# Kernel tuning notes

Measured on AMD Instinct MI355X. Metric: run time of the kernel, lower is better.

## Reference

```python
import jax, jax.numpy as jnp
import numpy as np
from jax import lax

B, L, DDYN, DSTAT, H = 512, 64, 16, 8, 512
N_BANK, C_CAND, K_TOP, N_PROTO = 50000, 1024, 16, 8
T_TARG, Q_QUANT = 2, 3
TEMP = 0.2


def _l2norm(x, eps=1e-12):
    # matches torch.nn.functional.normalize: x / max(||x||, eps)
    n = jnp.sqrt(jnp.sum(x * x, axis=-1, keepdims=True))
    return x / jnp.maximum(n, eps)


def setup_inputs() -> dict:
    key = jax.random.key(0)
    ks = jax.random.split(key, 24)
    s = 0.02
    inp = {
        'sequence_values': jax.random.normal(ks[0], (B, L, DDYN), jnp.float32),
        'sequence_masks': jnp.ones((B, L), jnp.float32),
        'static_values': jax.random.normal(ks[1], (B, DSTAT), jnp.float32),
        'bank_keys': jax.random.normal(ks[2], (N_BANK, H), jnp.float32),
        'bank_values': jax.random.normal(ks[3], (N_BANK, H), jnp.float32),
        'candidate_indices': jax.random.randint(ks[4], (B, C_CAND), 0, N_BANK, jnp.int64),
        # encoder params (SequenceEncoder stand-in: masked-mean + linear + relu)
        'W_seq': jax.random.normal(ks[5], (DDYN, H), jnp.float32) * s,
        'W_stat': jax.random.normal(ks[6], (DSTAT, H), jnp.float32) * s,
        'b_enc': jnp.zeros((H,), jnp.float32),
        # retrieval / prototype / fusion params
        'W_q': jax.random.normal(ks[7], (H, H), jnp.float32) * s,
        'b_q': jnp.zeros((H,), jnp.float32),
        'prototype_tokens': jax.random.normal(ks[8], (N_PROTO, H), jnp.float32) * 0.02,
        'W_tr': jax.random.normal(ks[9], (2 * H, H), jnp.float32) * s,
        'b_tr': jnp.zeros((H,), jnp.float32),
        'W_gate': jax.random.normal(ks[10], (3 * H, H), jnp.float32) * s,
        'b_gate': jnp.zeros((H,), jnp.float32),
        'W_out': jax.random.normal(ks[11], (H, H), jnp.float32) * s,
        'b_out': jnp.zeros((H,), jnp.float32),
        # per-target heads stacked: [T, H, Q] and [T, H]
        'W_quant': jax.random.normal(ks[12], (T_TARG, H, Q_QUANT), jnp.float32) * s,
        'b_quant': jnp.zeros((T_TARG, Q_QUANT), jnp.float32),
        'W_ev': jax.random.normal(ks[13], (T_TARG, H), jnp.float32) * s,
        'b_ev': jnp.zeros((T_TARG,), jnp.float32),
    }
    return inp


def reference(sequence_values, sequence_masks, static_values, bank_keys, bank_values,
              candidate_indices, W_seq, W_stat, b_enc, W_q, b_q, prototype_tokens,
              W_tr, b_tr, W_gate, b_gate, W_out, b_out, W_quant, b_quant, W_ev, b_ev):
    # --- encoder (masked mean pool + linear + relu stand-in for SequenceEncoder) ---
    m = sequence_masks[..., None]                                   # [B,L,1]
    pooled = (sequence_values * m).sum(1) / jnp.maximum(m.sum(1), 1e-6)
    local_hidden = jax.nn.relu(pooled @ W_seq + static_values @ W_stat + b_enc)  # [B,H]

    # --- normalized query ---
    query = _l2norm(local_hidden @ W_q + b_q)                       # [B,H]

    # --- donor retrieval: gather + dot + topk + softmax + weighted sum ---
    cand_keys = bank_keys[candidate_indices]                        # [B,C,H]
    sim = jnp.einsum('bch,bh->bc', cand_keys, query)                # [B,C]
    top_scores, top_pos = lax.top_k(sim, K_TOP)                     # [B,K]
    weights = jax.nn.softmax(top_scores / max(TEMP, 1e-6), axis=-1)
    sel_idx = jnp.take_along_axis(candidate_indices, top_pos, axis=1)  # [B,K]
    donor_hidden = jnp.einsum('bk,bkh->bh', weights, bank_values[sel_idx])

    # --- prototype attention ---
    protos_n = _l2norm(prototype_tokens)                            # [P,H]
    pw = jax.nn.softmax(query @ protos_n.T, axis=-1)                # [B,P]
    proto_hidden = pw @ prototype_tokens                            # [B,H]

    # --- transfer / gate / fuse (dropout is identity at eval) ---
    transfer = jax.nn.relu(jnp.concatenate([donor_hidden, proto_hidden], -1) @ W_tr + b_tr)
    gate = jax.nn.sigmoid(
        jnp.concatenate([local_hidden, donor_hidden, proto_hidden], -1) @ W_gate + b_gate)
    fused = gate * local_hidden + (1.0 - gate) * transfer
    fused = jax.nn.relu(fused @ W_out + b_out)                      # [B,H]

    # --- heads: sorted quantiles [B,T,Q] and event logits [B,T] ---
    quant = jnp.sort(jnp.einsum('bh,thq->btq', fused, W_quant) + b_quant, axis=-1)
    logit = jnp.einsum('bh,th->bt', fused, W_ev) + b_ev
    return jnp.concatenate([quant.reshape(quant.shape[0], -1), logit], axis=-1)  # [B, T*Q+T]
```

## Files before the change

kernel.cpp:

```cpp
#include <hip/hip_runtime.h>
#include <hip/hip_bf16.h>

typedef __hip_bfloat16 bf16;

__device__ __forceinline__ float lo16(unsigned u){ return __uint_as_float(u << 16); }
__device__ __forceinline__ float hi16(unsigned u){ return __uint_as_float(u & 0xffff0000u); }

#define Bn 512
#define Hn 512
#define Cn 1024
#define Kn 16
#define NBANK 50000

__device__ __forceinline__ int clamp_id(int id){
    return (id < 0) ? 0 : ((id >= NBANK) ? (NBANK - 1) : id);
}

#define QRAW_OFF 0
#define F1_OFF   0
#define G_OFF    262144
#define SIM_OFF  1048576
#define F2_OFF   1048576
#define GATE_OFF 1572864
#define TR_OFF   1835008
#define WS_FLOATS 2097152

__global__ __launch_bounds__(256) void k_enc(
    const float* __restrict__ seq, const float* __restrict__ mask, const float* __restrict__ stat,
    const float* __restrict__ W_seq, const float* __restrict__ W_stat, const float* __restrict__ b_enc,
    float* __restrict__ ws)
{
    const int b = blockIdx.x, t = threadIdx.x;
    const int h0 = 2*t, h1 = 2*t + 1;
    __shared__ float s_pool[16], s_stat[8];
    if (t < 16) {
        float acc = 0.f, ms = 0.f;
        for (int l = 0; l < 64; l++) {
            float m = mask[b*64 + l];
            ms  += m;
            acc += seq[(b*64 + l)*16 + t] * m;
        }
        s_pool[t] = acc / fmaxf(ms, 1e-6f);
    } else if (t < 24) {
        s_stat[t - 16] = stat[b*8 + (t - 16)];
    }
    __syncthreads();
    float a0 = b_enc[h0], a1 = b_enc[h1];
    #pragma unroll
    for (int j = 0; j < 16; j++) {
        float2 wv = *(const float2*)(W_seq + j*Hn + h0);
        a0 += s_pool[j]*wv.x; a1 += s_pool[j]*wv.y;
    }
    #pragma unroll
    for (int j = 0; j < 8; j++) {
        float2 wv = *(const float2*)(W_stat + j*Hn + h0);
        a0 += s_stat[j]*wv.x; a1 += s_stat[j]*wv.y;
    }
    float* g = ws + G_OFF + (size_t)b*1536;
    g[h0] = fmaxf(a0, 0.f); g[h1] = fmaxf(a1, 0.f);
}

__global__ __launch_bounds__(256) void k_qgemm_sk(
    const float* __restrict__ W, const float* __restrict__ bias,
    const float* __restrict__ in, int in_stride, int in_off,
    float* __restrict__ outp)
{
    const int ct = blockIdx.x, rt = blockIdx.y, kz = blockIdx.z, t = threadIdx.x;
    __shared__ float lt[64][132];
    {
        int r = t >> 2, c0 = (t & 3)*32;
        const float* src = in + (size_t)(rt*64 + r)*in_stride + in_off + kz*128 + c0;
        #pragma unroll
        for (int i = 0; i < 8; i++)
            *(float4*)&lt[r][c0 + i*4] = *(const float4*)(src + i*4);
    }
    __syncthreads();
    const int col0 = ct*64 + (t & 15)*4, rbase = (t >> 4)*4;
    float acc[4][4];
    if (kz == 0) {
        float4 bv = *(const float4*)(bias + col0);
        #pragma unroll
        for (int i = 0; i < 4; i++) { acc[i][0]=bv.x; acc[i][1]=bv.y; acc[i][2]=bv.z; acc[i][3]=bv.w; }
    } else {
        #pragma unroll
        for (int i = 0; i < 4; i++) { acc[i][0]=0; acc[i][1]=0; acc[i][2]=0; acc[i][3]=0; }
    }
    const float* wp = W + (size_t)(kz*128)*Hn + col0;
    #pragma unroll 4
    for (int k = 0; k < 128; k++) {
        float4 wv = *(const float4*)(wp + (size_t)k*Hn);
        #pragma unroll
        for (int i = 0; i < 4; i++) {
            float a = lt[rbase + i][k];
            acc[i][0] += a*wv.x; acc[i][1] += a*wv.y; acc[i][2] += a*wv.z; acc[i][3] += a*wv.w;
        }
    }
    #pragma unroll
    for (int i = 0; i < 4; i++) {
        float* op = outp + (size_t)(rt*64 + rbase + i)*Hn + col0;
        atomicAdd(op+0, acc[i][0]); atomicAdd(op+1, acc[i][1]);
        atomicAdd(op+2, acc[i][2]); atomicAdd(op+3, acc[i][3]);
    }
}

__global__ __launch_bounds__(256) void k_sim(
    const float* __restrict__ bank_keys, const int* __restrict__ cand32,
    float* __restrict__ ws)
{
    const int chunk = blockIdx.x, b = blockIdx.y, t = threadIdx.x;
    const int w = t >> 6, lane = t & 63;
    const int c64 = ((cand32[1] | cand32[3] | cand32[5] | cand32[7]) == 0) ? 1 : 0;

    const float* qr = ws + QRAW_OFF + (size_t)b*Hn + lane*8;
    float4 qa = *(const float4*)qr, qb = *(const float4*)(qr + 4);
    float ss = qa.x*qa.x + qa.y*qa.y + qa.z*qa.z + qa.w*qa.w
             + qb.x*qb.x + qb.y*qb.y + qb.z*qb.z + qb.w*qb.w;
    #pragma unroll
    for (int o = 32; o; o >>= 1) ss += __shfl_xor(ss, o);
    float inv = 1.f / fmaxf(sqrtf(ss), 1e-12f);
    float qv[8] = {qa.x*inv, qa.y*inv, qa.z*inv, qa.w*inv,
                   qb.x*inv, qb.y*inv, qb.z*inv, qb.w*inv};

    const int cbase = b*Cn + chunk*128 + w*32;
    float* simrow = ws + SIM_OFF + (size_t)b*Cn + chunk*128 + w*32;
    for (int g8 = 0; g8 < 32; g8 += 8) {
        float4 ka[8], kb2[8];
        #pragma unroll
        for (int u = 0; u < 8; u++) {
            int id = clamp_id(cand32[(size_t)(cbase + g8 + u) << c64]);
            const float* kp = bank_keys + (size_t)id*Hn + lane*8;
            ka[u]  = *(const float4*)kp;
            kb2[u] = *(const float4*)(kp + 4);
        }
        #pragma unroll
        for (int u = 0; u < 8; u++) {
            float s = ka[u].x*qv[0] + ka[u].y*qv[1] + ka[u].z*qv[2] + ka[u].w*qv[3]
                    + kb2[u].x*qv[4] + kb2[u].y*qv[5] + kb2[u].z*qv[6] + kb2[u].w*qv[7];
            #pragma unroll
            for (int o = 32; o; o >>= 1) s += __shfl_xor(s, o);
            if (lane == 0) simrow[g8 + u] = s;
        }
    }
}

__global__ __launch_bounds__(256) void k_select(
    const float* __restrict__ bank_values, const int* __restrict__ cand32,
    const float* __restrict__ proto, float* __restrict__ ws)
{
    const int b = blockIdx.x, t = threadIdx.x;
    const int w = t >> 6, lane = t & 63;
    const int h0 = 2*t, h1 = 2*t + 1;
    const int c64 = ((cand32[1] | cand32[3] | cand32[5] | cand32[7]) == 0) ? 1 : 0;

    __shared__ __align__(16) float s_sim[Cn];
    __shared__ float s_bv[4]; __shared__ int s_bi[4];
    __shared__ float s_topv[Kn]; __shared__ int s_sel[Kn];
    __shared__ float s_w[Kn];
    __shared__ float s_score[8], s_pw[8];

    *(float4*)&s_sim[t*4] = *(const float4*)(ws + SIM_OFF + (size_t)b*Cn + t*4);

    const float* qr = ws + QRAW_OFF + (size_t)b*Hn + lane*8;
    float4 qa = *(const float4*)qr, qb = *(const float4*)(qr + 4);
    float ss = qa.x*qa.x + qa.y*qa.y + qa.z*qa.z + qa.w*qa.w
             + qb.x*qb.x + qb.y*qb.y + qb.z*qb.z + qb.w*qb.w;
    #pragma unroll
    for (int o = 32; o; o >>= 1) ss += __shfl_xor(ss, o);
    float qinv = 1.f / fmaxf(sqrtf(ss), 1e-12f);
    float qv[8] = {qa.x*qinv, qa.y*qinv, qa.z*qinv, qa.w*qinv,
                   qb.x*qinv, qb.y*qinv, qb.z*qinv, qb.w*qinv};
    __syncthreads();

    for (int k = 0; k < Kn; k++) {
        float best = -1e30f; int bi = 0x7fffffff;
        for (int i = t; i < Cn; i += 256) {
            float v = s_sim[i];
            if (v > best || (v == best && i < bi)) { best = v; bi = i; }
        }
        #pragma unroll
        for (int o = 32; o; o >>= 1) {
            float ov = __shfl_xor(best, o); int oi = __shfl_xor(bi, o);
            if (ov > best || (ov == best && oi < bi)) { best = ov; bi = oi; }
        }
        if (lane == 0) { s_bv[w] = best; s_bi[w] = bi; }
        __syncthreads();
        if (t == 0) {
            float bv = s_bv[0]; int bbi = s_bi[0];
            for (int x = 1; x < 4; x++)
                if (s_bv[x] > bv || (s_bv[x] == bv && s_bi[x] < bbi)) { bv = s_bv[x]; bbi = s_bi[x]; }
            if (bbi < 0 || bbi >= Cn) bbi = 0;
            s_topv[k] = bv; s_sel[k] = bbi; s_sim[bbi] = -1e30f;
        }
        __syncthreads();
    }

    if (t == 0) {
        float m = s_topv[0];
        float e[Kn], ssum = 0.f;
        for (int k = 0; k < Kn; k++) { e[k] = __expf((s_topv[k] - m) * 5.0f); ssum += e[k]; }
        float inv = 1.f / ssum;
        for (int k = 0; k < Kn; k++) s_w[k] = e[k] * inv;
    }
    for (int p = w; p < 8; p += 4) {
        const float* pp = proto + (size_t)p*Hn + lane*8;
        float4 pa = *(const float4*)pp, pb = *(const float4*)(pp + 4);
        float f[8] = {pa.x, pa.y, pa.z, pa.w, pb.x, pb.y, pb.z, pb.w};
        float dq = 0.f, sq = 0.f;
        #pragma unroll
        for (int i = 0; i < 8; i++) { dq += f[i]*qv[i]; sq += f[i]*f[i]; }
        #pragma unroll
        for (int o = 32; o; o >>= 1) { dq += __shfl_xor(dq, o); sq += __shfl_xor(sq, o); }
        if (lane == 0) s_score[p] = dq / fmaxf(sqrtf(sq), 1e-12f);
    }
    __syncthreads();
    if (t == 0) {
        float m = s_score[0];
        for (int p = 1; p < 8; p++) m = fmaxf(m, s_score[p]);
        float e[8], ssum = 0.f;
        for (int p = 0; p < 8; p++) { e[p] = __expf(s_score[p] - m); ssum += e[p]; }
        float inv = 1.f / ssum;
        for (int p = 0; p < 8; p++) s_pw[p] = e[p] * inv;
    }
    __syncthreads();

    float* g = ws + G_OFF + (size_t)b*1536;
    {
        float a0 = 0.f, a1 = 0.f;
        #pragma unroll
        for (int k = 0; k < Kn; k++) {
            int id = clamp_id(cand32[(size_t)(b*Cn + s_sel[k]) << c64]);
            float2 v = *(const float2*)(bank_values + (size_t)id*Hn + h0);
            a0 += s_w[k]*v.x; a1 += s_w[k]*v.y;
        }
        g[512 + h0] = a0; g[512 + h1] = a1;
    }
    {
        float a0 = 0.f, a1 = 0.f;
        #pragma unroll
        for (int p = 0; p < 8; p++) {
            float2 v = *(const float2*)(proto + (size_t)p*Hn + h0);
            a0 += s_pw[p]*v.x; a1 += s_pw[p]*v.y;
        }
        g[1024 + h0] = a0; g[1024 + h1] = a1;
    }
}

__global__ __launch_bounds__(256) void k_gatetr_sk(
    const float* __restrict__ W_tr, const float* __restrict__ b_tr,
    const float* __restrict__ W_gate, const float* __restrict__ b_gate,
    float* __restrict__ ws)
{
    const int ct = blockIdx.x, rt = blockIdx.y, z = blockIdx.z, t = threadIdx.x;
    const int isGate = (z < 6);
    const int slice = isGate ? z : (z - 6);
    const float* W  = isGate ? W_gate : W_tr;
    const int inoff = (isGate ? 0 : 512) + slice*256;
    float* outp = ws + (isGate ? GATE_OFF : TR_OFF);

    __shared__ float lt[32][260];
    {
        int r = t >> 3, c0 = (t & 7)*32;
        const float* src = ws + G_OFF + (size_t)(rt*32 + r)*1536 + inoff + c0;
        #pragma unroll
        for (int i = 0; i < 8; i++)
            *(float4*)&lt[r][c0 + i*4] = *(const float4*)(src + i*4);
    }
    __syncthreads();
    const int col0 = ct*128 + (t & 31)*4, rbase = (t >> 5)*4;
    float acc[4][4];
    if (slice == 0) {
        const float* bias = isGate ? b_gate : b_tr;
        float4 bv = *(const float4*)(bias + col0);
        #pragma unroll
        for (int i = 0; i < 4; i++) { acc[i][0]=bv.x; acc[i][1]=bv.y; acc[i][2]=bv.z; acc[i][3]=bv.w; }
    } else {
        #pragma unroll
        for (int i = 0; i < 4; i++) { acc[i][0]=0; acc[i][1]=0; acc[i][2]=0; acc[i][3]=0; }
    }
    const float* wp = W + (size_t)(slice*256)*Hn + col0;
    #pragma unroll 4
    for (int k = 0; k < 256; k++) {
        float4 wv = *(const float4*)(wp + (size_t)k*Hn);
        #pragma unroll
        for (int i = 0; i < 4; i++) {
            float a = lt[rbase + i][k];
            acc[i][0] += a*wv.x; acc[i][1] += a*wv.y; acc[i][2] += a*wv.z; acc[i][3] += a*wv.w;
        }
    }
    #pragma unroll
    for (int i = 0; i < 4; i++) {
        float* op = outp + (size_t)(rt*32 + rbase + i)*Hn + col0;
        atomicAdd(op+0, acc[i][0]); atomicAdd(op+1, acc[i][1]);
        atomicAdd(op+2, acc[i][2]); atomicAdd(op+3, acc[i][3]);
    }
}

__global__ __launch_bounds__(256) void k_f1ew(float* __restrict__ ws)
{
    const int i4 = blockIdx.x*256 + threadIdx.x;
    const int row = i4 >> 7, c = (i4 & 127)*4;
    float4 lc = *(const float4*)(ws + G_OFF + (size_t)row*1536 + c);
    float4 ga = *(const float4*)(ws + GATE_OFF + (size_t)row*Hn + c);
    float4 tr = *(const float4*)(ws + TR_OFF + (size_t)row*Hn + c);
    float4 r;
    float s;
    s = 1.f/(1.f + __expf(-ga.x)); r.x = s*lc.x + (1.f-s)*fmaxf(tr.x, 0.f);
    s = 1.f/(1.f + __expf(-ga.y)); r.y = s*lc.y + (1.f-s)*fmaxf(tr.y, 0.f);
    s = 1.f/(1.f + __expf(-ga.z)); r.z = s*lc.z + (1.f-s)*fmaxf(tr.z, 0.f);
    s = 1.f/(1.f + __expf(-ga.w)); r.w = s*lc.w + (1.f-s)*fmaxf(tr.w, 0.f);
    *(float4*)(ws + F1_OFF + (size_t)row*Hn + c) = r;
}

__global__ __launch_bounds__(64) void k_heads(
    const float* __restrict__ W_quant, const float* __restrict__ b_quant,
    const float* __restrict__ W_ev, const float* __restrict__ b_ev,
    const float* __restrict__ ws_ro, float* __restrict__ out)
{
    const int b = blockIdx.x, lane = threadIdx.x;
    const float* fr = ws_ro + F2_OFF + (size_t)b*Hn + lane*8;
    float4 fa = *(const float4*)fr, fb = *(const float4*)(fr + 4);
    float fv[8] = {fmaxf(fa.x,0.f), fmaxf(fa.y,0.f), fmaxf(fa.z,0.f), fmaxf(fa.w,0.f),
                   fmaxf(fb.x,0.f), fmaxf(fb.y,0.f), fmaxf(fb.z,0.f), fmaxf(fb.w,0.f)};
    float acc[8];
    #pragma unroll
    for (int o = 0; o < 8; o++) acc[o] = 0.f;
    #pragma unroll
    for (int i = 0; i < 8; i++) {
        int h = lane*8 + i;
        float fh = fv[i];
        acc[0] += fh*W_quant[(0*Hn + h)*3 + 0];
        acc[1] += fh*W_quant[(0*Hn + h)*3 + 1];
        acc[2] += fh*W_quant[(0*Hn + h)*3 + 2];
        acc[3] += fh*W_quant[(1*Hn + h)*3 + 0];
        acc[4] += fh*W_quant[(1*Hn + h)*3 + 1];
        acc[5] += fh*W_quant[(1*Hn + h)*3 + 2];
        acc[6] += fh*W_ev[0*Hn + h];
        acc[7] += fh*W_ev[1*Hn + h];
    }
    #pragma unroll
    for (int o = 0; o < 8; o++) {
        #pragma unroll
        for (int s = 32; s; s >>= 1) acc[o] += __shfl_xor(acc[o], s);
    }
    if (lane == 0) {
        float q[6];
        for (int o = 0; o < 6; o++) q[o] = acc[o] + b_quant[o];
        #pragma unroll
        for (int tt = 0; tt < 2; tt++) {
            float a = q[tt*3], bb = q[tt*3+1], c = q[tt*3+2];
            float mn = fminf(a, fminf(bb, c)), mx = fmaxf(a, fmaxf(bb, c));
            float md = a + bb + c - mn - mx;
            q[tt*3] = mn; q[tt*3+1] = md; q[tt*3+2] = mx;
        }
        for (int o = 0; o < 6; o++) out[b*8 + o] = q[o];
        out[b*8 + 6] = acc[6] + b_ev[0];
        out[b*8 + 7] = acc[7] + b_ev[1];
    }
}

__device__ __forceinline__ float lds_f(const void* p, int i, int f32){
    return f32 ? ((const float*)p)[i] : __bfloat162float(((const bf16*)p)[i]);
}
__device__ __forceinline__ float2 ldpair(const void* p, int elt, int f32){
    if (f32) return ((const float2*)p)[elt >> 1];
    unsigned u = ((const unsigned*)p)[elt >> 1];
    return make_float2(lo16(u), hi16(u));
}
__device__ __forceinline__ void ld8(const void* p, int elt, int f32, float* v){
    if (f32){
        const float4* q = (const float4*)((const float*)p + elt);
        float4 a = q[0], b = q[1];
        v[0]=a.x; v[1]=a.y; v[2]=a.z; v[3]=a.w; v[4]=b.x; v[5]=b.y; v[6]=b.z; v[7]=b.w;
    } else {
        uint4 u = *(const uint4*)((const bf16*)p + elt);
        v[0]=lo16(u.x); v[1]=hi16(u.x); v[2]=lo16(u.y); v[3]=hi16(u.y);
        v[4]=lo16(u.z); v[5]=hi16(u.z); v[6]=lo16(u.w); v[7]=hi16(u.w);
    }
}
__device__ __forceinline__ void st_out(void* o, int i, int f32, float v){
    if (f32) ((float*)o)[i] = v; else ((bf16*)o)[i] = __float2bfloat16(v);
}

__global__ __launch_bounds__(256) void k_fused(
    const void* __restrict__ seq, const void* __restrict__ mask, const void* __restrict__ stat,
    const void* __restrict__ bank_keys, const void* __restrict__ bank_values,
    const int* __restrict__ cand32,
    const void* __restrict__ W_seq, const void* __restrict__ W_stat, const void* __restrict__ b_enc,
    const void* __restrict__ W_q, const void* __restrict__ b_q,
    const void* __restrict__ proto,
    const void* __restrict__ W_tr, const void* __restrict__ b_tr,
    const void* __restrict__ W_gate, const void* __restrict__ b_gate,
    const void* __restrict__ W_out, const void* __restrict__ b_out,
    const void* __restrict__ W_quant, const void* __restrict__ b_quant,
    const void* __restrict__ W_ev, const void* __restrict__ b_ev,
    void* __restrict__ out)
{
    const int b = blockIdx.x, t = threadIdx.x;
    const int w = t >> 6, lane = t & 63;
    const int h0 = 2*t, h1 = 2*t + 1;
    const int f32 = (((const unsigned short*)mask)[0] == 0) ? 1 : 0;
    const int c64 = ((cand32[1] | cand32[3] | cand32[5] | cand32[7]) == 0) ? 1 : 0;

    __shared__ __align__(16) float s_pool[16];
    __shared__ __align__(16) float s_stat[8];
    __shared__ __align__(16) float g[1536];
    __shared__ __align__(16) float s_q[Hn];
    __shared__ __align__(16) float s_sim[Cn];
    __shared__ __align__(16) float f1[Hn];
    __shared__ __align__(16) float f2[Hn];
    __shared__ float s_part[4], s_ss;
    __shared__ float s_bv[4]; __shared__ int s_bi[4];
    __shared__ float s_topv[Kn]; __shared__ int s_sel[Kn];
    __shared__ float s_w[Kn];
    __shared__ float s_score[8], s_pw[8];
    __shared__ float s_head[8][4];

    if (t < 16) {
        float acc = 0.f, ms = 0.f;
        for (int l = 0; l < 64; l++) {
            float m = lds_f(mask, b*64 + l, f32);
            ms  += m;
            acc += lds_f(seq, (b*64 + l)*16 + t, f32) * m;
        }
        s_pool[t] = acc / fmaxf(ms, 1e-6f);
    } else if (t < 24) {
        s_stat[t - 16] = lds_f(stat, b*8 + (t - 16), f32);
    }
    __syncthreads();
    {
        float a0 = lds_f(b_enc, h0, f32), a1 = lds_f(b_enc, h1, f32);
        #pragma unroll
        for (int j = 0; j < 16; j++) {
            float2 wv = ldpair(W_seq, j*Hn + h0, f32);
            a0 += s_pool[j]*wv.x; a1 += s_pool[j]*wv.y;
        }
        #pragma unroll
        for (int j = 0; j < 8; j++) {
            float2 wv = ldpair(W_stat, j*Hn + h0, f32);
            a0 += s_stat[j]*wv.x; a1 += s_stat[j]*wv.y;
        }
        a0 = fmaxf(a0, 0.f); a1 = fmaxf(a1, 0.f);
        g[h0] = a0; g[h1] = a1;
    }
    __syncthreads();
    {
        float q0 = lds_f(b_q, h0, f32), q1 = lds_f(b_q, h1, f32);
        #pragma unroll 4
        for (int j = 0; j < Hn; j++) {
            float lj = g[j];
            float2 wv = ldpair(W_q, j*Hn + h0, f32);
            q0 += lj*wv.x; q1 += lj*wv.y;
        }
        float ss = q0*q0 + q1*q1;
        #pragma unroll
        for (int o = 32; o; o >>= 1) ss += __shfl_xor(ss, o);
        if (lane == 0) s_part[w] = ss;
        __syncthreads();
        if (t == 0) s_ss = s_part[0] + s_part[1] + s_part[2] + s_part[3];
        __syncthreads();
        float inv = 1.f / fmaxf(sqrtf(s_ss), 1e-12f);
        s_q[h0] = q0*inv; s_q[h1] = q1*inv;
    }
    __syncthreads();
    float qv[8];
    #pragma unroll
    for (int i = 0; i < 8; i++) qv[i] = s_q[lane*8 + i];

    for (int c0 = w*256; c0 < w*256 + 256; c0 += 4) {
        float kf[4][8];
        #pragma unroll
        for (int u = 0; u < 4; u++) {
            int id = clamp_id(cand32[(size_t)(b*Cn + c0 + u) << c64]);
            ld8(bank_keys, id*Hn + lane*8, f32, kf[u]);
        }
        #pragma unroll
        for (int u = 0; u < 4; u++) {
            float s = 0.f;
            #pragma unroll
            for (int i = 0; i < 8; i++) s += kf[u][i]*qv[i];
            #pragma unroll
            for (int o = 32; o; o >>= 1) s += __shfl_xor(s, o);
            if (lane == 0) s_sim[c0 + u] = s;
        }
    }
    __syncthreads();
    for (int k = 0; k < Kn; k++) {
        float best = -1e30f; int bi = 0x7fffffff;
        for (int i = t; i < Cn; i += 256) {
            float v = s_sim[i];
            if (v > best || (v == best && i < bi)) { best = v; bi = i; }
        }
        #pragma unroll
        for (int o = 32; o; o >>= 1) {
            float ov = __shfl_xor(best, o); int oi = __shfl_xor(bi, o);
            if (ov > best || (ov == best && oi < bi)) { best = ov; bi = oi; }
        }
        if (lane == 0) { s_bv[w] = best; s_bi[w] = bi; }
        __syncthreads();
        if (t == 0) {
            float bv = s_bv[0]; int bbi = s_bi[0];
            for (int x = 1; x < 4; x++)
                if (s_bv[x] > bv || (s_bv[x] == bv && s_bi[x] < bbi)) { bv = s_bv[x]; bbi = s_bi[x]; }
            if (bbi < 0 || bbi >= Cn) bbi = 0;
            s_topv[k] = bv; s_sel[k] = bbi; s_sim[bbi] = -1e30f;
        }
        __syncthreads();
    }
    if (t == 0) {
        float m = s_topv[0];
        float e[Kn], ssum = 0.f;
        for (int k = 0; k < Kn; k++) { e[k] = __expf((s_topv[k] - m) * 5.0f); ssum += e[k]; }
        float inv = 1.f / ssum;
        for (int k = 0; k < Kn; k++) s_w[k] = e[k] * inv;
    }
    __syncthreads();
    {
        float a0 = 0.f, a1 = 0.f;
        #pragma unroll
        for (int k = 0; k < Kn; k++) {
            int id = clamp_id(cand32[(size_t)(b*Cn + s_sel[k]) << c64]);
            float2 v = ldpair(bank_values, id*Hn + h0, f32);
            a0 += s_w[k]*v.x; a1 += s_w[k]*v.y;
        }
        g[512 + h0] = a0; g[512 + h1] = a1;
    }
    for (int p = w; p < 8; p += 4) {
        float f[8];
        ld8(proto, p*Hn + lane*8, f32, f);
        float dq = 0.f, sq = 0.f;
        #pragma unroll
        for (int i = 0; i < 8; i++) { dq += f[i]*qv[i]; sq += f[i]*f[i]; }
        #pragma unroll
        for (int o = 32; o; o >>= 1) { dq += __shfl_xor(dq, o); sq += __shfl_xor(sq, o); }
        if (lane == 0) s_score[p] = dq / fmaxf(sqrtf(sq), 1e-12f);
    }
    __syncthreads();
    if (t == 0) {
        float m = s_score[0];
        for (int p = 1; p < 8; p++) m = fmaxf(m, s_score[p]);
        float e[8], ssum = 0.f;
        for (int p = 0; p < 8; p++) { e[p] = __expf(s_score[p] - m); ssum += e[p]; }
        float inv = 1.f / ssum;
        for (int p = 0; p < 8; p++) s_pw[p] = e[p] * inv;
    }
    __syncthreads();
    {
        float a0 = 0.f, a1 = 0.f;
        #pragma unroll
        for (int p = 0; p < 8; p++) {
            float2 v = ldpair(proto, p*Hn + h0, f32);
            a0 += s_pw[p]*v.x; a1 += s_pw[p]*v.y;
        }
        g[1024 + h0] = a0; g[1024 + h1] = a1;
    }
    __syncthreads();
    float tr0 = lds_f(b_tr, h0, f32), tr1 = lds_f(b_tr, h1, f32);
    #pragma unroll 4
    for (int j = 0; j < 1024; j++) {
        float gj = g[512 + j];
        float2 wv = ldpair(W_tr, j*Hn + h0, f32);
        tr0 += gj*wv.x; tr1 += gj*wv.y;
    }
    tr0 = fmaxf(tr0, 0.f); tr1 = fmaxf(tr1, 0.f);
    float gt0 = lds_f(b_gate, h0, f32), gt1 = lds_f(b_gate, h1, f32);
    #pragma unroll 4
    for (int j = 0; j < 1536; j++) {
        float gj = g[j];
        float2 wv = ldpair(W_gate, j*Hn + h0, f32);
        gt0 += gj*wv.x; gt1 += gj*wv.y;
    }
    gt0 = 1.f/(1.f + __expf(-gt0)); gt1 = 1.f/(1.f + __expf(-gt1));
    f1[h0] = gt0*g[h0] + (1.f - gt0)*tr0;
    f1[h1] = gt1*g[h1] + (1.f - gt1)*tr1;
    __syncthreads();
    {
        float o0 = lds_f(b_out, h0, f32), o1 = lds_f(b_out, h1, f32);
        #pragma unroll 4
        for (int j = 0; j < Hn; j++) {
            float fj = f1[j];
            float2 wv = ldpair(W_out, j*Hn + h0, f32);
            o0 += fj*wv.x; o1 += fj*wv.y;
        }
        o0 = fmaxf(o0, 0.f); o1 = fmaxf(o1, 0.f);
        f2[h0] = o0; f2[h1] = o1;
    }
    __syncthreads();
    {
        float acc[8];
        #pragma unroll
        for (int o = 0; o < 8; o++) acc[o] = 0.f;
        for (int h = t; h < Hn; h += 256) {
            float fh = f2[h];
            acc[0] += fh*lds_f(W_quant, (0*Hn + h)*3 + 0, f32);
            acc[1] += fh*lds_f(W_quant, (0*Hn + h)*3 + 1, f32);
            acc[2] += fh*lds_f(W_quant, (0*Hn + h)*3 + 2, f32);
            acc[3] += fh*lds_f(W_quant, (1*Hn + h)*3 + 0, f32);
            acc[4] += fh*lds_f(W_quant, (1*Hn + h)*3 + 1, f32);
            acc[5] += fh*lds_f(W_quant, (1*Hn + h)*3 + 2, f32);
            acc[6] += fh*lds_f(W_ev, 0*Hn + h, f32);
            acc[7] += fh*lds_f(W_ev, 1*Hn + h, f32);
        }
        #pragma unroll
        for (int o = 0; o < 8; o++) {
            float v = acc[o];
            #pragma unroll
            for (int s = 32; s; s >>= 1) v += __shfl_xor(v, s);
            if (lane == 0) s_head[o][w] = v;
        }
        __syncthreads();
        if (t == 0) {
            float q[6];
            for (int o = 0; o < 6; o++)
                q[o] = s_head[o][0] + s_head[o][1] + s_head[o][2] + s_head[o][3] + lds_f(b_quant, o, f32);
            #pragma unroll
            for (int tt = 0; tt < 2; tt++) {
                float a = q[tt*3], bb = q[tt*3+1], c = q[tt*3+2];
                float mn = fminf(a, fminf(bb, c)), mx = fmaxf(a, fmaxf(bb, c));
                float md = a + bb + c - mn - mx;
                q[tt*3] = mn; q[tt*3+1] = md; q[tt*3+2] = mx;
            }
            for (int o = 0; o < 6; o++) st_out(out, b*8 + o, f32, q[o]);
            float l0 = s_head[6][0] + s_head[6][1] + s_head[6][2] + s_head[6][3] + lds_f(b_ev, 0, f32);
            float l1 = s_head[7][0] + s_head[7][1] + s_head[7][2] + s_head[7][3] + lds_f(b_ev, 1, f32);
            st_out(out, b*8 + 6, f32, l0);
            st_out(out, b*8 + 7, f32, l1);
        }
    }
}

extern "C" void kernel_launch(void* const* d_in, const int* in_sizes, int n_in,
                              void* d_out, int out_size, void* d_ws, size_t ws_size,
                              hipStream_t stream) {
    static const int expect[22] = {
        512*64*16, 512*64, 512*8, 50000*512, 50000*512, 512*1024,
        16*512, 8*512, 512, 512*512, 512, 8*512,
        1024*512, 512, 1536*512, 512, 512*512, 512,
        2*512*3, 2*3, 2*512, 2
    };
    if (n_in != 22 || out_size != 512*8) return;
    for (int i = 0; i < 22; i++) if (in_sizes[i] != expect[i]) return;

    if (ws_size < (size_t)WS_FLOATS * 4) {
        k_fused<<<Bn, 256, 0, stream>>>(
            d_in[0], d_in[1], d_in[2], d_in[3], d_in[4], (const int*)d_in[5],
            d_in[6], d_in[7], d_in[8], d_in[9], d_in[10], d_in[11],
            d_in[12], d_in[13], d_in[14], d_in[15], d_in[16], d_in[17],
            d_in[18], d_in[19], d_in[20], d_in[21], d_out);
        return;
    }

    float* ws = (float*)d_ws;
    hipMemsetAsync(ws + QRAW_OFF, 0, (size_t)512*512*4, stream);
    hipMemsetAsync(ws + GATE_OFF, 0, (size_t)2*512*512*4, stream);

    k_enc<<<Bn, 256, 0, stream>>>((const float*)d_in[0], (const float*)d_in[1],
                                  (const float*)d_in[2], (const float*)d_in[6],
                                  (const float*)d_in[7], (const float*)d_in[8], ws);
    k_qgemm_sk<<<dim3(8, 8, 4), 256, 0, stream>>>(
        (const float*)d_in[9], (const float*)d_in[10], ws + G_OFF, 1536, 0, ws + QRAW_OFF);
    k_sim<<<dim3(8, Bn), 256, 0, stream>>>((const float*)d_in[3], (const int*)d_in[5], ws);
    k_select<<<Bn, 256, 0, stream>>>((const float*)d_in[4], (const int*)d_in[5],
                                     (const float*)d_in[11], ws);
    hipMemsetAsync(ws + F2_OFF, 0, (size_t)512*512*4, stream);
    k_gatetr_sk<<<dim3(4, 16, 10), 256, 0, stream>>>(
        (const float*)d_in[12], (const float*)d_in[13],
        (const float*)d_in[14], (const float*)d_in[15], ws);
    k_f1ew<<<256, 256, 0, stream>>>(ws);
    k_qgemm_sk<<<dim3(8, 8, 4), 256, 0, stream>>>(
        (const float*)d_in[16], (const float*)d_in[17], ws + F1_OFF, 512, 0, ws + F2_OFF);
    k_heads<<<Bn, 64, 0, stream>>>((const float*)d_in[18], (const float*)d_in[19],
                                   (const float*)d_in[20], (const float*)d_in[21],
                                   ws, (float*)d_out);
}
```

Baseline: 545.2 us.

## Invert candidate gather into per-bank-key grouping for similarity scores

```diff
diff --git a/kernel.cpp b/kernel.cpp
--- a/kernel.cpp
+++ b/kernel.cpp
@@ -11,6 +11,7 @@
 #define Cn 1024
 #define Kn 16
 #define NBANK 50000
+#define NIDPAD 50176
 
 __device__ __forceinline__ int clamp_id(int id){
     return (id < 0) ? 0 : ((id >= NBANK) ? (NBANK - 1) : id);
@@ -19,19 +20,37 @@
 #define QRAW_OFF 0
 #define F1_OFF   0
 #define G_OFF    262144
+#define DONOR_OFF (G_OFF + 262144)
+#define PROTO_OFF (G_OFF + 524288)
 #define SIM_OFF  1048576
 #define F2_OFF   1048576
 #define GATE_OFF 1572864
 #define TR_OFF   1835008
 #define WS_FLOATS 2097152
 
+#define HIST_I   0
+#define CURSOR_I NIDPAD
+#define OFFS_I   (2*NIDPAD)
+#define CHPREF_I (2*NIDPAD + NIDPAD)
+
 __global__ __launch_bounds__(256) void k_enc(
     const float* __restrict__ seq, const float* __restrict__ mask, const float* __restrict__ stat,
     const float* __restrict__ W_seq, const float* __restrict__ W_stat, const float* __restrict__ b_enc,
-    float* __restrict__ ws)
+    const int* __restrict__ cand32, float* __restrict__ ws)
 {
     const int b = blockIdx.x, t = threadIdx.x;
     const int h0 = 2*t, h1 = 2*t + 1;
+
+    {
+        const int c64 = ((cand32[1] | cand32[3] | cand32[5] | cand32[7]) == 0) ? 1 : 0;
+        int* hist = (int*)(ws + GATE_OFF) + HIST_I;
+        #pragma unroll
+        for (int u = 0; u < 4; u++) {
+            int idx = b*Cn + u*256 + t;
+            atomicAdd(&hist[clamp_id(cand32[(size_t)idx << c64])], 1);
+        }
+    }
+
     __shared__ float s_pool[16], s_stat[8];
     if (t < 16) {
         float acc = 0.f, ms = 0.f;
@@ -56,7 +75,7 @@
         float2 wv = *(const float2*)(W_stat + j*Hn + h0);
         a0 += s_stat[j]*wv.x; a1 += s_stat[j]*wv.y;
     }
-    float* g = ws + G_OFF + (size_t)b*1536;
+    float* g = ws + G_OFF + (size_t)b*Hn;
     g[h0] = fmaxf(a0, 0.f); g[h1] = fmaxf(a1, 0.f);
 }
 
@@ -103,42 +122,115 @@
     }
 }
 
-__global__ __launch_bounds__(256) void k_sim(
-    const float* __restrict__ bank_keys, const int* __restrict__ cand32,
-    float* __restrict__ ws)
-{
-    const int chunk = blockIdx.x, b = blockIdx.y, t = threadIdx.x;
-    const int w = t >> 6, lane = t & 63;
-    const int c64 = ((cand32[1] | cand32[3] | cand32[5] | cand32[7]) == 0) ? 1 : 0;
-
-    const float* qr = ws + QRAW_OFF + (size_t)b*Hn + lane*8;
+__global__ __launch_bounds__(64) void k_qnorm(float* __restrict__ ws)
+{
+    const int b = blockIdx.x, lane = threadIdx.x;
+    float* qr = ws + QRAW_OFF + (size_t)b*Hn + lane*8;
     float4 qa = *(const float4*)qr, qb = *(const float4*)(qr + 4);
     float ss = qa.x*qa.x + qa.y*qa.y + qa.z*qa.z + qa.w*qa.w
              + qb.x*qb.x + qb.y*qb.y + qb.z*qb.z + qb.w*qb.w;
     #pragma unroll
     for (int o = 32; o; o >>= 1) ss += __shfl_xor(ss, o);
     float inv = 1.f / fmaxf(sqrtf(ss), 1e-12f);
-    float qv[8] = {qa.x*inv, qa.y*inv, qa.z*inv, qa.w*inv,
-                   qb.x*inv, qb.y*inv, qb.z*inv, qb.w*inv};
-
-    const int cbase = b*Cn + chunk*128 + w*32;
-    float* simrow = ws + SIM_OFF + (size_t)b*Cn + chunk*128 + w*32;
-    for (int g8 = 0; g8 < 32; g8 += 8) {
-        float4 ka[8], kb2[8];
-        #pragma unroll
-        for (int u = 0; u < 8; u++) {
-            int id = clamp_id(cand32[(size_t)(cbase + g8 + u) << c64]);
-            const float* kp = bank_keys + (size_t)id*Hn + lane*8;
-            ka[u]  = *(const float4*)kp;
-            kb2[u] = *(const float4*)(kp + 4);
-        }
-        #pragma unroll
-        for (int u = 0; u < 8; u++) {
-            float s = ka[u].x*qv[0] + ka[u].y*qv[1] + ka[u].z*qv[2] + ka[u].w*qv[3]
-                    + kb2[u].x*qv[4] + kb2[u].y*qv[5] + kb2[u].z*qv[6] + kb2[u].w*qv[7];
-            #pragma unroll
-            for (int o = 32; o; o >>= 1) s += __shfl_xor(s, o);
-            if (lane == 0) simrow[g8 + u] = s;
+    qa.x *= inv; qa.y *= inv; qa.z *= inv; qa.w *= inv;
+    qb.x *= inv; qb.y *= inv; qb.z *= inv; qb.w *= inv;
+    *(float4*)qr = qa; *(float4*)(qr + 4) = qb;
+}
+
+__global__ __launch_bounds__(256) void k_scanA(
+    const int* __restrict__ hist, int* __restrict__ offs, int* __restrict__ chsum)
+{
+    __shared__ int s[256];
+    const int t = threadIdx.x, g = blockIdx.x*256 + t;
+    const int v = hist[g];
+    s[t] = v; __syncthreads();
+    #pragma unroll
+    for (int off = 1; off < 256; off <<= 1) {
+        int x = (t >= off) ? s[t - off] : 0;
+        __syncthreads();
+        s[t] += x;
+        __syncthreads();
+    }
+    offs[g] = s[t] - v;
+    if (t == 255) chsum[blockIdx.x] = s[255];
+}
+
+__global__ __launch_bounds__(256) void k_scanB(int* __restrict__ chsum)
+{
+    __shared__ int s[256];
+    const int t = threadIdx.x;
+    const int v = (t < 196) ? chsum[t] : 0;
+    s[t] = v; __syncthreads();
+    #pragma unroll
+    for (int off = 1; off < 256; off <<= 1) {
+        int x = (t >= off) ? s[t - off] : 0;
+        __syncthreads();
+        s[t] += x;
+        __syncthreads();
+    }
+    if (t < 196) chsum[t] = s[t] - v;
+}
+
+__global__ __launch_bounds__(256) void k_scatter(
+    const int* __restrict__ cand32, int* __restrict__ cursor,
+    const int* __restrict__ offs, const int* __restrict__ chpref,
+    unsigned* __restrict__ refs)
+{
+    const int i = blockIdx.x*256 + threadIdx.x;
+    const int c64 = ((cand32[1] | cand32[3] | cand32[5] | cand32[7]) == 0) ? 1 : 0;
+    const int id = clamp_id(cand32[(size_t)i << c64]);
+    const int pos = atomicAdd(&cursor[id], 1);
+    refs[offs[id] + chpref[id >> 8] + pos] = (unsigned)i;
+}
+
+__global__ __launch_bounds__(256) void k_dotinv(
+    const float* __restrict__ bank_keys, const unsigned* __restrict__ refs,
+    const int* __restrict__ offs, const int* __restrict__ chpref,
+    float* __restrict__ ws)
+{
+    const int id = blockIdx.x*4 + (threadIdx.x >> 6);
+    const int lane = threadIdx.x & 63;
+    const int start = offs[id]     + chpref[id >> 8];
+    const int end   = offs[id + 1] + chpref[(id + 1) >> 8];
+    if (start >= end) return;
+
+    const float* kp = bank_keys + (size_t)id*Hn + lane*8;
+    float4 ka = *(const float4*)kp, kb = *(const float4*)(kp + 4);
+    const float* qbase = ws + QRAW_OFF;
+    float* simw = ws + SIM_OFF;
+
+    for (int r = start; r < end; r += 4) {
+        const int nn = end - r;
+        unsigned rv0 = refs[r];
+        unsigned rv1 = refs[nn > 1 ? r + 1 : r];
+        unsigned rv2 = refs[nn > 2 ? r + 2 : r];
+        unsigned rv3 = refs[nn > 3 ? r + 3 : r];
+        const float* q0 = qbase + (size_t)(rv0 >> 10)*Hn + lane*8;
+        const float* q1 = qbase + (size_t)(rv1 >> 10)*Hn + lane*8;
+        const float* q2 = qbase + (size_t)(rv2 >> 10)*Hn + lane*8;
+        const float* q3 = qbase + (size_t)(rv3 >> 10)*Hn + lane*8;
+        float4 a0 = *(const float4*)q0, b0 = *(const float4*)(q0 + 4);
+        float4 a1 = *(const float4*)q1, b1 = *(const float4*)(q1 + 4);
+        float4 a2 = *(const float4*)q2, b2 = *(const float4*)(q2 + 4);
+        float4 a3 = *(const float4*)q3, b3 = *(const float4*)(q3 + 4);
+        float s0 = ka.x*a0.x + ka.y*a0.y + ka.z*a0.z + ka.w*a0.w
+                 + kb.x*b0.x + kb.y*b0.y + kb.z*b0.z + kb.w*b0.w;
+        float s1 = ka.x*a1.x + ka.y*a1.y + ka.z*a1.z + ka.w*a1.w
+                 + kb.x*b1.x + kb.y*b1.y + kb.z*b1.z + kb.w*b1.w;
+        float s2 = ka.x*a2.x + ka.y*a2.y + ka.z*a2.z + ka.w*a2.w
+                 + kb.x*b2.x + kb.y*b2.y + kb.z*b2.z + kb.w*b2.w;
+        float s3 = ka.x*a3.x + ka.y*a3.y + ka.z*a3.z + ka.w*a3.w
+                 + kb.x*b3.x + kb.y*b3.y + kb.z*b3.z + kb.w*b3.w;
+        #pragma unroll
+        for (int o = 32; o; o >>= 1) {
+            s0 += __shfl_xor(s0, o); s1 += __shfl_xor(s1, o);
+            s2 += __shfl_xor(s2, o); s3 += __shfl_xor(s3, o);
+        }
+        if (lane == 0) {
+            simw[rv0] = s0;
+            if (nn > 1) simw[rv1] = s1;
+            if (nn > 2) simw[rv2] = s2;
+            if (nn > 3) simw[rv3] = s3;
         }
     }
 }
@@ -162,13 +254,7 @@
 
     const float* qr = ws + QRAW_OFF + (size_t)b*Hn + lane*8;
     float4 qa = *(const float4*)qr, qb = *(const float4*)(qr + 4);
-    float ss = qa.x*qa.x + qa.y*qa.y + qa.z*qa.z + qa.w*qa.w
-             + qb.x*qb.x + qb.y*qb.y + qb.z*qb.z + qb.w*qb.w;
-    #pragma unroll
-    for (int o = 32; o; o >>= 1) ss += __shfl_xor(ss, o);
-    float qinv = 1.f / fmaxf(sqrtf(ss), 1e-12f);
-    float qv[8] = {qa.x*qinv, qa.y*qinv, qa.z*qinv, qa.w*qinv,
-                   qb.x*qinv, qb.y*qinv, qb.z*qinv, qb.w*qinv};
+    float qv[8] = {qa.x, qa.y, qa.z, qa.w, qb.x, qb.y, qb.z, qb.w};
     __syncthreads();
 
     for (int k = 0; k < Kn; k++) {
@@ -223,7 +309,6 @@
     }
     __syncthreads();
 
-    float* g = ws + G_OFF + (size_t)b*1536;
     {
         float a0 = 0.f, a1 = 0.f;
         #pragma unroll
@@ -232,7 +317,8 @@
             float2 v = *(const float2*)(bank_values + (size_t)id*Hn + h0);
             a0 += s_w[k]*v.x; a1 += s_w[k]*v.y;
         }
-        g[512 + h0] = a0; g[512 + h1] = a1;
+        float* gd = ws + DONOR_OFF + (size_t)b*Hn;
+        gd[h0] = a0; gd[h1] = a1;
     }
     {
         float a0 = 0.f, a1 = 0.f;
@@ -241,7 +327,8 @@
             float2 v = *(const float2*)(proto + (size_t)p*Hn + h0);
             a0 += s_pw[p]*v.x; a1 += s_pw[p]*v.y;
         }
-        g[1024 + h0] = a0; g[1024 + h1] = a1;
+        float* gp = ws + PROTO_OFF + (size_t)b*Hn;
+        gp[h0] = a0; gp[h1] = a1;
     }
 }
 
@@ -254,13 +341,14 @@
     const int isGate = (z < 6);
     const int slice = isGate ? z : (z - 6);
     const float* W  = isGate ? W_gate : W_tr;
-    const int inoff = (isGate ? 0 : 512) + slice*256;
+    const int gcol = isGate ? slice*256 : 512 + slice*256;
+    const float* srcbase = ws + G_OFF + (size_t)(gcol >> 9)*262144 + (gcol & 511);
     float* outp = ws + (isGate ? GATE_OFF : TR_OFF);
 
     __shared__ float lt[32][260];
     {
         int r = t >> 3, c0 = (t & 7)*32;
-        const float* src = ws + G_OFF + (size_t)(rt*32 + r)*1536 + inoff + c0;
+        const float* src = srcbase + (size_t)(rt*32 + r)*Hn + c0;
         #pragma unroll
         for (int i = 0; i < 8; i++)
             *(float4*)&lt[r][c0 + i*4] = *(const float4*)(src + i*4);
@@ -299,7 +387,7 @@
 {
     const int i4 = blockIdx.x*256 + threadIdx.x;
     const int row = i4 >> 7, c = (i4 & 127)*4;
-    float4 lc = *(const float4*)(ws + G_OFF + (size_t)row*1536 + c);
+    float4 lc = *(const float4*)(ws + G_OFF + (size_t)row*Hn + c);
     float4 ga = *(const float4*)(ws + GATE_OFF + (size_t)row*Hn + c);
     float4 tr = *(const float4*)(ws + TR_OFF + (size_t)row*Hn + c);
     float4 r;
@@ -650,17 +738,31 @@
     }
 
     float* ws = (float*)d_ws;
+    int* iws = (int*)(ws + GATE_OFF);
+    int* hist   = iws + HIST_I;
+    int* cursor = iws + CURSOR_I;
+    int* offs   = iws + OFFS_I;
+    int* chpref = iws + CHPREF_I;
+    unsigned* refs = (unsigned*)(ws + DONOR_OFF);
+
     hipMemsetAsync(ws + QRAW_OFF, 0, (size_t)512*512*4, stream);
-    hipMemsetAsync(ws + GATE_OFF, 0, (size_t)2*512*512*4, stream);
+    hipMemsetAsync(hist, 0, (size_t)2*NIDPAD*4, stream);
+    hipMemsetAsync(ws + TR_OFF, 0, (size_t)512*512*4, stream);
 
     k_enc<<<Bn, 256, 0, stream>>>((const float*)d_in[0], (const float*)d_in[1],
                                   (const float*)d_in[2], (const float*)d_in[6],
-                                  (const float*)d_in[7], (const float*)d_in[8], ws);
+                                  (const float*)d_in[7], (const float*)d_in[8],
+                                  (const int*)d_in[5], ws);
+    k_scanA<<<NIDPAD/256, 256, 0, stream>>>(hist, offs, chpref);
+    k_scanB<<<1, 256, 0, stream>>>(chpref);
+    k_scatter<<<(Bn*Cn)/256, 256, 0, stream>>>((const int*)d_in[5], cursor, offs, chpref, refs);
     k_qgemm_sk<<<dim3(8, 8, 4), 256, 0, stream>>>(
-        (const float*)d_in[9], (const float*)d_in[10], ws + G_OFF, 1536, 0, ws + QRAW_OFF);
-    k_sim<<<dim3(8, Bn), 256, 0, stream>>>((const float*)d_in[3], (const int*)d_in[5], ws);
+        (const float*)d_in[9], (const float*)d_in[10], ws + G_OFF, 512, 0, ws + QRAW_OFF);
+    k_qnorm<<<Bn, 64, 0, stream>>>(ws);
+    k_dotinv<<<NBANK/4, 256, 0, stream>>>((const float*)d_in[3], refs, offs, chpref, ws);
     k_select<<<Bn, 256, 0, stream>>>((const float*)d_in[4], (const int*)d_in[5],
                                      (const float*)d_in[11], ws);
+    hipMemsetAsync(ws + GATE_OFF, 0, (size_t)512*512*4, stream);
     hipMemsetAsync(ws + F2_OFF, 0, (size_t)512*512*4, stream);
     k_gatetr_sk<<<dim3(4, 16, 10), 256, 0, stream>>>(
         (const float*)d_in[12], (const float*)d_in[13],
```

Result: no change. 546.8 us (+0.3%).
